# Kernel tuning notes

Hardware: AMD Instinct MI355X
Metric: run time of the kernel (lower is better)

## Reference

```python
import jax, jax.numpy as jnp
import numpy as np

N = 50000   # nodes
E = 800000  # edges (avg degree 16)
C = 96      # in = hidden = out channels


def setup_inputs() -> dict:
    key = jax.random.key(0)
    ks = jax.random.split(key, 8)
    s = np.float32(1.0 / np.sqrt(C))
    x = jax.random.normal(ks[0], (N, C), dtype=jnp.float32)
    edge_index = jax.random.randint(ks[1], (2, E), 0, N, dtype=jnp.int64)
    W1 = jax.random.normal(ks[2], (C, C), dtype=jnp.float32) * s
    Wr1 = jax.random.normal(ks[3], (C, C), dtype=jnp.float32) * s
    b1 = jnp.zeros((C,), dtype=jnp.float32)
    W2 = jax.random.normal(ks[4], (C, C), dtype=jnp.float32) * s
    Wr2 = jax.random.normal(ks[5], (C, C), dtype=jnp.float32) * s
    b2 = jnp.zeros((C,), dtype=jnp.float32)
    return {"x": x, "edge_index": edge_index,
            "W1": W1, "Wr1": Wr1, "b1": b1,
            "W2": W2, "Wr2": Wr2, "b2": b2}


def spline_conv(x, edge_index, W, W_root, b):
    """Gather-transform-scatter message passing (SplineConv core, mean aggr)."""
    src, dst = edge_index[0], edge_index[1]
    h = x @ W                                   # [N, C] transform once per node
    msg = h[src]                                # [E, C] edge gather
    agg = jax.ops.segment_sum(msg, dst, num_segments=N)        # scatter-add
    deg = jax.ops.segment_sum(jnp.ones((E,), x.dtype), dst, num_segments=N)
    agg = agg / jnp.maximum(deg, 1.0)[:, None]  # mean aggregation
    return agg + x @ W_root + b                 # root weight + bias


def reference(x, edge_index, W1, Wr1, b1, W2, Wr2, b2):
    h = jax.nn.relu(spline_conv(x, edge_index, W1, Wr1, b1))
    out = spline_conv(h, edge_index, W2, Wr2, b2)
    return out.reshape(-1)  # generalization of x.view(1600)
```

## Files before the change

### kernel.cpp

```cpp
#include <hip/hip_runtime.h>

#define C 96
#define TB 64
#define EB 2048
#define NBP 1024
#define LCAP 2048
typedef unsigned char u8;
typedef unsigned short u16;
typedef unsigned int u32;
typedef __attribute__((ext_vector_type(8))) short short8;
typedef __attribute__((ext_vector_type(4))) float floatx4;
typedef __attribute__((ext_vector_type(2))) float floatx2;

__device__ inline u16 f2bf(float f) {
    union { float f; u32 u; } v; v.f = f;
    u32 r = v.u + 0x7fff + ((v.u >> 16) & 1);
    return (u16)(r >> 16);
}
__device__ inline u32 pk4_fp8(float a, float b, float c, float d) {
    u32 w = 0;
    w = __builtin_amdgcn_cvt_pk_fp8_f32(a, b, w, false);
    w = __builtin_amdgcn_cvt_pk_fp8_f32(c, d, w, true);
    return w;
}
__device__ inline u8 f2fp8(float a) {
    return (u8)(__builtin_amdgcn_cvt_pk_fp8_f32(a, a, 0, false) & 0xff);
}

__global__ __launch_bounds__(256) void sort_kernel(const int* __restrict__ src,
                                                   const int* __restrict__ dst,
                                                   int* __restrict__ cntT,
                                                   int* __restrict__ offT,
                                                   u32* __restrict__ stage,
                                                   int E, int DB, int NB,
                                                   const float* __restrict__ x,
                                                   u16* __restrict__ xb,
                                                   u8* __restrict__ xf8, int n16, int CX,
                                                   const float* W0, const float* W1,
                                                   const float* W2, const float* W3,
                                                   u16* T0, u16* T1, u16* T2, u16* T3) {
    int bid = blockIdx.x;
    int t = threadIdx.x;
    if (bid >= DB) {
        int cc = bid - DB;
        if (cc < CX) {
            int i = cc * 256 + t;
            if (i >= n16) return;
            const float4* p = (const float4*)x + (size_t)i * 4;
            float4 a = p[0], b = p[1], c = p[2], d = p[3];
            short8 o0, o1;
            o0[0] = (short)f2bf(a.x); o0[1] = (short)f2bf(a.y);
            o0[2] = (short)f2bf(a.z); o0[3] = (short)f2bf(a.w);
            o0[4] = (short)f2bf(b.x); o0[5] = (short)f2bf(b.y);
            o0[6] = (short)f2bf(b.z); o0[7] = (short)f2bf(b.w);
            o1[0] = (short)f2bf(c.x); o1[1] = (short)f2bf(c.y);
            o1[2] = (short)f2bf(c.z); o1[3] = (short)f2bf(c.w);
            o1[4] = (short)f2bf(d.x); o1[5] = (short)f2bf(d.y);
            o1[6] = (short)f2bf(d.z); o1[7] = (short)f2bf(d.w);
            *(short8*)(xb + (size_t)i * 16) = o0;
            *(short8*)(xb + (size_t)i * 16 + 8) = o1;
            uint4 f8;
            f8.x = pk4_fp8(a.x, a.y, a.z, a.w);
            f8.y = pk4_fp8(b.x, b.y, b.z, b.w);
            f8.z = pk4_fp8(c.x, c.y, c.z, c.w);
            f8.w = pk4_fp8(d.x, d.y, d.z, d.w);
            *(uint4*)(xf8 + (size_t)i * 16) = f8;
        } else {
            int w = cc - CX;
            const float* W = w == 0 ? W0 : w == 1 ? W1 : w == 2 ? W2 : W3;
            u16* T = w == 0 ? T0 : w == 1 ? T1 : w == 2 ? T2 : T3;
            for (int i = t; i < C * C; i += 256) {
                int k = i / C, n = i - k * C;
                T[n * C + k] = f2bf(W[i]);
            }
        }
        return;
    }

    __shared__ u32 s_word[EB];
    __shared__ int s_cnt[NBP];
    __shared__ int s_off[NBP];
    __shared__ int s_scan[256];
    int e0 = bid * EB;
    int cnt_here = min(EB, E - e0);

    for (int i = t; i < NBP; i += 256) s_cnt[i] = 0;
    __syncthreads();

    int my_src[EB / 256], my_dl[EB / 256], my_b[EB / 256], my_rank[EB / 256];
    int nmine = 0;
#pragma unroll
    for (int k = 0; k < EB / 256; k++) {
        int i = t + k * 256;
        if (i < cnt_here) {
            int s = src[e0 + i], d = dst[e0 + i];
            int b = d >> 6;
            my_src[nmine] = s;
            my_dl[nmine] = d & (TB - 1);
            my_b[nmine] = b;
            my_rank[nmine] = atomicAdd(&s_cnt[b], 1);
            nmine++;
        }
    }
    __syncthreads();

    int b4 = t * 4;
    int v0 = s_cnt[b4], v1 = s_cnt[b4 + 1], v2 = s_cnt[b4 + 2], v3 = s_cnt[b4 + 3];
    int lsum = v0 + v1 + v2 + v3;
    s_scan[t] = lsum;
    __syncthreads();
    for (int off = 1; off < 256; off <<= 1) {
        int x2 = (t >= off) ? s_scan[t - off] : 0;
        __syncthreads();
        s_scan[t] += x2;
        __syncthreads();
    }
    int excl = s_scan[t] - lsum;
    s_off[b4] = excl;
    s_off[b4 + 1] = excl + v0;
    s_off[b4 + 2] = excl + v0 + v1;
    s_off[b4 + 3] = excl + v0 + v1 + v2;
    __syncthreads();

    for (int b = t; b < NB; b += 256) {
        cntT[(size_t)b * DB + bid] = s_cnt[b];
        offT[(size_t)b * DB + bid] = s_off[b];
    }

    for (int k = 0; k < nmine; k++) {
        int slot = s_off[my_b[k]] + my_rank[k];
        s_word[slot] = ((u32)my_dl[k] << 16) | (u32)my_src[k];
    }
    __syncthreads();

    for (int i = t; i < cnt_here; i += 256) stage[(size_t)bid * EB + i] = s_word[i];
}

template <bool RELU, bool WF8, typename OT>
__global__ __launch_bounds__(256, 4) void layer_kernel(const u16* __restrict__ Xbf,
                                                       const u8* __restrict__ Xf8,
                                                       const int* __restrict__ cntT,
                                                       const int* __restrict__ offT,
                                                       const u32* __restrict__ stage,
                                                       const u16* __restrict__ WTA,
                                                       const u16* __restrict__ WTR,
                                                       const float* __restrict__ BIAS,
                                                       OT* __restrict__ Y,
                                                       u8* __restrict__ Yf8, int n, int DB) {
    __shared__ __align__(16) u16 sA[64 * 104];
    __shared__ u16 lcsr[LCAP];
    __shared__ int s_cnt64[TB];
    __shared__ int s_off64[TB];
    __shared__ int s_cur64[TB];
    __shared__ int s_perm[TB];
    const int t = threadIdx.x;
    const int b = blockIdx.x;
    const int row0 = b * 64;
    const int* cntT_b = cntT + (size_t)b * DB;
    const int* offT_b = offT + (size_t)b * DB;

    for (int i = t; i < TB; i += 256) s_cnt64[i] = 0;
    __syncthreads();
    for (int i = t; i < DB; i += 256) {
        int len = cntT_b[i];
        const u32* run = stage + (size_t)i * EB + offT_b[i];
        for (int j = 0; j < len; j++) atomicAdd(&s_cnt64[run[j] >> 16], 1);
    }
    __syncthreads();

    int dv = (t < TB) ? s_cnt64[t] : 0;
    if (t < TB) s_cur64[t] = dv;
    __syncthreads();
    for (int off = 1; off < TB; off <<= 1) {
        int x2 = (t >= off && t < TB) ? s_cur64[t - off] : 0;
        __syncthreads();
        if (t < TB) s_cur64[t] += x2;
        __syncthreads();
    }
    if (t < TB) {
        int excl = s_cur64[t] - dv;
        s_off64[t] = excl;
    }
    __syncthreads();
    if (t < TB) s_cur64[t] = s_off64[t];
    __syncthreads();

    for (int i = t; i < DB; i += 256) {
        int len = cntT_b[i];
        const u32* run = stage + (size_t)i * EB + offT_b[i];
        for (int j = 0; j < len; j++) {
            u32 w = run[j];
            int p = atomicAdd(&s_cur64[w >> 16], 1);
            lcsr[p] = (u16)(w & 0xffffu);
        }
    }
    __syncthreads();

    if (t < 64) {
        int di = s_cnt64[t];
        int r = 0;
#pragma unroll 8
        for (int j = 0; j < 64; j++) {
            int dj = s_cnt64[j];
            r += (dj < di) || (dj == di && j < t);
        }
        s_perm[r] = t;
    }
    __syncthreads();

    {
        int nl = s_perm[t >> 2];
        int q = t & 3;
        float acc[24];
#pragma unroll
        for (int i = 0; i < 24; i++) acc[i] = 0.f;
        int d = s_cnt64[nl];
        int start = s_off64[nl];
        const int off4 = q * 16;
        const int off2 = 64 + q * 8;

        int j = 0;
        if (d >= 4) {
            int si[4];
#pragma unroll
            for (int k = 0; k < 4; k++) si[k] = lcsr[start + k];
            for (; j + 8 <= d; j += 4) {
                uint4 va[4];
                uint2 vb[4];
#pragma unroll
                for (int k = 0; k < 4; k++) {
                    const u8* p = Xf8 + (size_t)si[k] * 96;
                    va[k] = *(const uint4*)(p + off4);
                    vb[k] = *(const uint2*)(p + off2);
                }
                int sn[4];
#pragma unroll
                for (int k = 0; k < 4; k++) sn[k] = lcsr[start + j + 4 + k];
#pragma unroll
                for (int k = 0; k < 4; k++) {
                    u32 ws[6] = {va[k].x, va[k].y, va[k].z,
                                 va[k].w, vb[k].x, vb[k].y};
#pragma unroll
                    for (int i = 0; i < 6; i++) {
                        floatx2 lo = __builtin_amdgcn_cvt_pk_f32_fp8(ws[i], false);
                        floatx2 hi = __builtin_amdgcn_cvt_pk_f32_fp8(ws[i], true);
                        acc[4 * i]     += lo[0];
                        acc[4 * i + 1] += lo[1];
                        acc[4 * i + 2] += hi[0];
                        acc[4 * i + 3] += hi[1];
                    }
                }
#pragma unroll
                for (int k = 0; k < 4; k++) si[k] = sn[k];
            }
            {
                uint4 va[4];
                uint2 vb[4];
#pragma unroll
                for (int k = 0; k < 4; k++) {
                    const u8* p = Xf8 + (size_t)si[k] * 96;
                    va[k] = *(const uint4*)(p + off4);
                    vb[k] = *(const uint2*)(p + off2);
                }
#pragma unroll
                for (int k = 0; k < 4; k++) {
                    u32 ws[6] = {va[k].x, va[k].y, va[k].z,
                                 va[k].w, vb[k].x, vb[k].y};
#pragma unroll
                    for (int i = 0; i < 6; i++) {
                        floatx2 lo = __builtin_amdgcn_cvt_pk_f32_fp8(ws[i], false);
                        floatx2 hi = __builtin_amdgcn_cvt_pk_f32_fp8(ws[i], true);
                        acc[4 * i]     += lo[0];
                        acc[4 * i + 1] += lo[1];
                        acc[4 * i + 2] += hi[0];
                        acc[4 * i + 3] += hi[1];
                    }
                }
                j += 4;
            }
        }
        for (; j < d; j++) {
            const u8* p = Xf8 + (size_t)lcsr[start + j] * 96;
            uint4 va = *(const uint4*)(p + off4);
            uint2 vb = *(const uint2*)(p + off2);
            u32 ws[6] = {va.x, va.y, va.z, va.w, vb.x, vb.y};
#pragma unroll
            for (int i = 0; i < 6; i++) {
                floatx2 lo = __builtin_amdgcn_cvt_pk_f32_fp8(ws[i], false);
                floatx2 hi = __builtin_amdgcn_cvt_pk_f32_fp8(ws[i], true);
                acc[4 * i]     += lo[0];
                acc[4 * i + 1] += lo[1];
                acc[4 * i + 2] += hi[0];
                acc[4 * i + 3] += hi[1];
            }
        }
        float inv = 1.0f / fmaxf((float)d, 1.0f);
        u16* dl = sA + nl * 104;
        short8 o0, o1, o2;
#pragma unroll
        for (int i = 0; i < 8; i++) {
            o0[i] = (short)f2bf(acc[i] * inv);
            o1[i] = (short)f2bf(acc[8 + i] * inv);
            o2[i] = (short)f2bf(acc[16 + i] * inv);
        }
        *(short8*)(dl + q * 16) = o0;
        *(short8*)(dl + q * 16 + 8) = o1;
        *(short8*)(dl + 64 + q * 8) = o2;
    }
    __syncthreads();

    const int lane = t & 63;
    const int w = t >> 6;
    const int quad = lane >> 4;
    const int l16 = lane & 15;
    const int r0 = row0 + w * 16;

    floatx4 acc6[6];
#pragma unroll
    for (int i = 0; i < 6; i++) acc6[i] = (floatx4){0.f, 0.f, 0.f, 0.f};

    {
        const u16* Ap = sA + (w * 16 + l16) * 104 + quad * 8;
        const u16* Wp = WTA + l16 * C + quad * 8;
#pragma unroll
        for (int ks = 0; ks < 3; ks++) {
            short8 a = *(const short8*)(Ap + ks * 32);
#pragma unroll
            for (int nt = 0; nt < 6; nt++) {
                short8 bb = *(const short8*)(Wp + nt * 16 * C + ks * 32);
                acc6[nt] = __builtin_amdgcn_mfma_f32_16x16x32_bf16(a, bb, acc6[nt], 0, 0, 0);
            }
        }
    }
    {
        int arow = r0 + l16;
        if (arow >= n) arow = n - 1;
        const u16* Xp = Xbf + (size_t)arow * C + quad * 8;
        const u16* Wp = WTR + l16 * C + quad * 8;
#pragma unroll
        for (int ks = 0; ks < 3; ks++) {
            short8 a = *(const short8*)(Xp + ks * 32);
#pragma unroll
            for (int nt = 0; nt < 6; nt++) {
                short8 bb = *(const short8*)(Wp + nt * 16 * C + ks * 32);
                acc6[nt] = __builtin_amdgcn_mfma_f32_16x16x32_bf16(a, bb, acc6[nt], 0, 0, 0);
            }
        }
    }

#pragma unroll
    for (int nt = 0; nt < 6; nt++) {
        float bv = BIAS[nt * 16 + l16];
#pragma unroll
        for (int r = 0; r < 4; r++) {
            float v = acc6[nt][r] + bv;
            if (RELU) v = fmaxf(v, 0.f);
            acc6[nt][r] = v;
        }
    }
    __syncthreads();

    const int nrow = min(64, n - row0);
    const int lr = w * 16 + quad * 4;

    if constexpr (sizeof(OT) == 2) {
        u16* so = sA;
#pragma unroll
        for (int nt = 0; nt < 6; nt++)
#pragma unroll
            for (int r = 0; r < 4; r++)
                so[(lr + r) * 96 + nt * 16 + l16] = f2bf(acc6[nt][r]);
        __syncthreads();
        {
            char* dstp = (char*)Y + (size_t)row0 * 192;
            int nbytes = nrow * 192;
            for (int ofs = t * 16; ofs < nbytes; ofs += 4096)
                *(uint4*)(dstp + ofs) = *(const uint4*)((const char*)sA + ofs);
        }
        if constexpr (WF8) {
            __syncthreads();
            u8* so8 = (u8*)sA;
#pragma unroll
            for (int nt = 0; nt < 6; nt++)
#pragma unroll
                for (int r = 0; r < 4; r++)
                    so8[(lr + r) * 96 + nt * 16 + l16] = f2fp8(acc6[nt][r]);
            __syncthreads();
            char* dst8 = (char*)Yf8 + (size_t)row0 * 96;
            int nb8 = nrow * 96;
            for (int ofs = t * 16; ofs < nb8; ofs += 4096)
                *(uint4*)(dst8 + ofs) = *(const uint4*)((const char*)sA + ofs);
        }
    } else {
        float* sof = (float*)sA;
#pragma unroll
        for (int half = 0; half < 2; half++) {
            if (half) __syncthreads();
            if ((w >> 1) == half) {
#pragma unroll
                for (int nt = 0; nt < 6; nt++)
#pragma unroll
                    for (int r = 0; r < 4; r++)
                        sof[((w & 1) * 16 + quad * 4 + r) * 96 + nt * 16 + l16] = acc6[nt][r];
            }
            __syncthreads();
            int rbase = row0 + half * 32;
            int nr = n - rbase;
            nr = nr < 0 ? 0 : (nr > 32 ? 32 : nr);
            char* dstp = (char*)Y + (size_t)rbase * 384;
            int nbytes = nr * 384;
            for (int ofs = t * 16; ofs < nbytes; ofs += 4096)
                *(uint4*)(dstp + ofs) = *(const uint4*)((const char*)sA + ofs);
        }
    }
}

extern "C" void kernel_launch(void* const* d_in, const int* in_sizes, int n_in,
                              void* d_out, int out_size, void* d_ws, size_t ws_size,
                              hipStream_t stream) {
    const float* x   = (const float*)d_in[0];
    const int*   ei  = (const int*)d_in[1];
    const float* W1  = (const float*)d_in[2];
    const float* Wr1 = (const float*)d_in[3];
    const float* b1  = (const float*)d_in[4];
    const float* W2  = (const float*)d_in[5];
    const float* Wr2 = (const float*)d_in[6];
    const float* b2  = (const float*)d_in[7];
    float* out = (float*)d_out;

    const int N = in_sizes[0] / C;
    const int E = in_sizes[1] / 2;
    const int* src = ei;
    const int* dst = ei + E;

    const int DB   = (E + EB - 1) / EB;
    const int NB   = (N + TB - 1) / TB;
    const int n16  = N * C / 16;
    const int CX   = (n16 + 255) / 256;
    const size_t NBDB = ((size_t)NB * DB + 3) & ~(size_t)3;

    int*  cntT = (int*)d_ws;
    int*  offT = cntT + NBDB;
    u32*  stage = (u32*)(offT + NBDB);
    u16*  xb   = (u16*)(stage + (size_t)DB * EB);
    u16*  h1b  = xb + (size_t)N * C;
    u16*  wt   = h1b + (size_t)N * C;
    u16 *wt1 = wt, *wtr1 = wt + C * C, *wt2 = wt + 2 * C * C, *wtr2 = wt + 3 * C * C;
    u8*   xf8  = (u8*)(wt + 4 * C * C);
    u8*   h1f8 = xf8 + (size_t)N * 96;

    sort_kernel<<<DB + CX + 4, 256, 0, stream>>>(src, dst, cntT, offT, stage,
                                                 E, DB, NB,
                                                 x, xb, xf8, n16, CX,
                                                 W1, Wr1, W2, Wr2, wt1, wtr1, wt2, wtr2);

    layer_kernel<true, true, u16><<<NB, 256, 0, stream>>>(
        xb, xf8, cntT, offT, stage, wt1, wtr1, b1, h1b, h1f8, N, DB);
    layer_kernel<false, false, float><<<NB, 256, 0, stream>>>(
        h1b, h1f8, cntT, offT, stage, wt2, wtr2, b2, out, h1f8, N, DB);
}
```

Measured before the change: 169.5 us.

## Pack count/offset table and read staged edge runs once into shared memory

```diff
diff --git a/kernel.cpp b/kernel.cpp
--- a/kernel.cpp
+++ b/kernel.cpp
@@ -29,8 +29,7 @@
 
 __global__ __launch_bounds__(256) void sort_kernel(const int* __restrict__ src,
                                                    const int* __restrict__ dst,
-                                                   int* __restrict__ cntT,
-                                                   int* __restrict__ offT,
+                                                   u32* __restrict__ tabT,
                                                    u32* __restrict__ stage,
                                                    int E, int DB, int NB,
                                                    const float* __restrict__ x,
@@ -122,10 +121,8 @@
     s_off[b4 + 3] = excl + v0 + v1 + v2;
     __syncthreads();
 
-    for (int b = t; b < NB; b += 256) {
-        cntT[(size_t)b * DB + bid] = s_cnt[b];
-        offT[(size_t)b * DB + bid] = s_off[b];
-    }
+    for (int b = t; b < NB; b += 256)
+        tabT[(size_t)b * DB + bid] = ((u32)s_cnt[b] << 16) | (u32)s_off[b];
 
     for (int k = 0; k < nmine; k++) {
         int slot = s_off[my_b[k]] + my_rank[k];
@@ -137,10 +134,9 @@
 }
 
 template <bool RELU, bool WF8, typename OT>
-__global__ __launch_bounds__(256, 4) void layer_kernel(const u16* __restrict__ Xbf,
+__global__ __launch_bounds__(256, 6) void layer_kernel(const u16* __restrict__ Xbf,
                                                        const u8* __restrict__ Xf8,
-                                                       const int* __restrict__ cntT,
-                                                       const int* __restrict__ offT,
+                                                       const u32* __restrict__ tabT,
                                                        const u32* __restrict__ stage,
                                                        const u16* __restrict__ WTA,
                                                        const u16* __restrict__ WTR,
@@ -149,26 +145,49 @@
                                                        u8* __restrict__ Yf8, int n, int DB) {
     __shared__ __align__(16) u16 sA[64 * 104];
     __shared__ u16 lcsr[LCAP];
-    __shared__ int s_cnt64[TB];
+    __shared__ int s_dg[TB];
     __shared__ int s_off64[TB];
     __shared__ int s_cur64[TB];
     __shared__ int s_perm[TB];
+    __shared__ int ssum[256];
+    u32* raw = (u32*)sA;
     const int t = threadIdx.x;
     const int b = blockIdx.x;
     const int row0 = b * 64;
-    const int* cntT_b = cntT + (size_t)b * DB;
-    const int* offT_b = offT + (size_t)b * DB;
-
-    for (int i = t; i < TB; i += 256) s_cnt64[i] = 0;
-    __syncthreads();
-    for (int i = t; i < DB; i += 256) {
-        int len = cntT_b[i];
-        const u32* run = stage + (size_t)i * EB + offT_b[i];
-        for (int j = 0; j < len; j++) atomicAdd(&s_cnt64[run[j] >> 16], 1);
-    }
-    __syncthreads();
-
-    int dv = (t < TB) ? s_cnt64[t] : 0;
+    const u32* tab_b = tabT + (size_t)b * DB;
+
+    for (int i = t; i < TB; i += 256) s_dg[i] = 0;
+    u32 p0 = (t < DB) ? tab_b[t] : 0;
+    u32 p1 = (t + 256 < DB) ? tab_b[t + 256] : 0;
+    int l0 = p0 >> 16, o0 = p0 & 0xffff;
+    int l1 = p1 >> 16, o1 = p1 & 0xffff;
+    int tot = l0 + l1;
+    ssum[t] = tot;
+    __syncthreads();
+    for (int off = 1; off < 256; off <<= 1) {
+        int x2 = (t >= off) ? ssum[t - off] : 0;
+        __syncthreads();
+        ssum[t] += x2;
+        __syncthreads();
+    }
+    const int seg0 = ssum[t] - tot;
+    int pos = seg0;
+    {
+        const u32* run = stage + (size_t)t * EB + o0;
+        for (int j = 0; j < l0; j++) {
+            u32 w = run[j];
+            if (pos < LCAP) { raw[pos++] = w; atomicAdd(&s_dg[w >> 16], 1); }
+        }
+        const u32* run2 = stage + ((size_t)t + 256) * EB + o1;
+        for (int j = 0; j < l1; j++) {
+            u32 w = run2[j];
+            if (pos < LCAP) { raw[pos++] = w; atomicAdd(&s_dg[w >> 16], 1); }
+        }
+    }
+    const int stored = pos - seg0;
+    __syncthreads();
+
+    int dv = (t < TB) ? s_dg[t] : 0;
     if (t < TB) s_cur64[t] = dv;
     __syncthreads();
     for (int off = 1; off < TB; off <<= 1) {
@@ -177,31 +196,24 @@
         if (t < TB) s_cur64[t] += x2;
         __syncthreads();
     }
-    if (t < TB) {
-        int excl = s_cur64[t] - dv;
-        s_off64[t] = excl;
-    }
+    if (t < TB) s_off64[t] = s_cur64[t] - dv;
     __syncthreads();
     if (t < TB) s_cur64[t] = s_off64[t];
     __syncthreads();
 
-    for (int i = t; i < DB; i += 256) {
-        int len = cntT_b[i];
-        const u32* run = stage + (size_t)i * EB + offT_b[i];
-        for (int j = 0; j < len; j++) {
-            u32 w = run[j];
-            int p = atomicAdd(&s_cur64[w >> 16], 1);
-            lcsr[p] = (u16)(w & 0xffffu);
-        }
+    for (int k = 0; k < stored; k++) {
+        u32 w = raw[seg0 + k];
+        int p = atomicAdd(&s_cur64[w >> 16], 1);
+        lcsr[p] = (u16)(w & 0xffffu);
     }
     __syncthreads();
 
     if (t < 64) {
-        int di = s_cnt64[t];
+        int di = s_dg[t];
         int r = 0;
 #pragma unroll 8
         for (int j = 0; j < 64; j++) {
-            int dj = s_cnt64[j];
+            int dj = s_dg[j];
             r += (dj < di) || (dj == di && j < t);
         }
         s_perm[r] = t;
@@ -214,98 +226,72 @@
         float acc[24];
 #pragma unroll
         for (int i = 0; i < 24; i++) acc[i] = 0.f;
-        int d = s_cnt64[nl];
+        int d = s_dg[nl];
         int start = s_off64[nl];
         const int off4 = q * 16;
         const int off2 = 64 + q * 8;
 
+#define CONSUME(va, vb)                                                     \
+        do {                                                                \
+            u32 ws[6] = {(va).x, (va).y, (va).z, (va).w, (vb).x, (vb).y};   \
+            _Pragma("unroll")                                               \
+            for (int i = 0; i < 6; i++) {                                   \
+                floatx2 lo = __builtin_amdgcn_cvt_pk_f32_fp8(ws[i], false); \
+                floatx2 hi = __builtin_amdgcn_cvt_pk_f32_fp8(ws[i], true);  \
+                acc[4 * i]     += lo[0];                                    \
+                acc[4 * i + 1] += lo[1];                                    \
+                acc[4 * i + 2] += hi[0];                                    \
+                acc[4 * i + 3] += hi[1];                                    \
+            }                                                               \
+        } while (0)
+
         int j = 0;
-        if (d >= 4) {
-            int si[4];
-#pragma unroll
-            for (int k = 0; k < 4; k++) si[k] = lcsr[start + k];
-            for (; j + 8 <= d; j += 4) {
-                uint4 va[4];
-                uint2 vb[4];
-#pragma unroll
-                for (int k = 0; k < 4; k++) {
-                    const u8* p = Xf8 + (size_t)si[k] * 96;
-                    va[k] = *(const uint4*)(p + off4);
-                    vb[k] = *(const uint2*)(p + off2);
-                }
-                int sn[4];
-#pragma unroll
-                for (int k = 0; k < 4; k++) sn[k] = lcsr[start + j + 4 + k];
-#pragma unroll
-                for (int k = 0; k < 4; k++) {
-                    u32 ws[6] = {va[k].x, va[k].y, va[k].z,
-                                 va[k].w, vb[k].x, vb[k].y};
-#pragma unroll
-                    for (int i = 0; i < 6; i++) {
-                        floatx2 lo = __builtin_amdgcn_cvt_pk_f32_fp8(ws[i], false);
-                        floatx2 hi = __builtin_amdgcn_cvt_pk_f32_fp8(ws[i], true);
-                        acc[4 * i]     += lo[0];
-                        acc[4 * i + 1] += lo[1];
-                        acc[4 * i + 2] += hi[0];
-                        acc[4 * i + 3] += hi[1];
-                    }
-                }
-#pragma unroll
-                for (int k = 0; k < 4; k++) si[k] = sn[k];
+        if (d >= 2) {
+            int si0 = lcsr[start], si1 = lcsr[start + 1];
+            for (; j + 4 <= d; j += 2) {
+                const u8* pA = Xf8 + (size_t)si0 * 96;
+                const u8* pB = Xf8 + (size_t)si1 * 96;
+                uint4 va0 = *(const uint4*)(pA + off4);
+                uint2 vb0 = *(const uint2*)(pA + off2);
+                uint4 va1 = *(const uint4*)(pB + off4);
+                uint2 vb1 = *(const uint2*)(pB + off2);
+                si0 = lcsr[start + j + 2];
+                si1 = lcsr[start + j + 3];
+                CONSUME(va0, vb0);
+                CONSUME(va1, vb1);
             }
             {
-                uint4 va[4];
-                uint2 vb[4];
-#pragma unroll
-                for (int k = 0; k < 4; k++) {
-                    const u8* p = Xf8 + (size_t)si[k] * 96;
-                    va[k] = *(const uint4*)(p + off4);
-                    vb[k] = *(const uint2*)(p + off2);
-                }
-#pragma unroll
-                for (int k = 0; k < 4; k++) {
-                    u32 ws[6] = {va[k].x, va[k].y, va[k].z,
-                                 va[k].w, vb[k].x, vb[k].y};
-#pragma unroll
-                    for (int i = 0; i < 6; i++) {
-                        floatx2 lo = __builtin_amdgcn_cvt_pk_f32_fp8(ws[i], false);
-                        floatx2 hi = __builtin_amdgcn_cvt_pk_f32_fp8(ws[i], true);
-                        acc[4 * i]     += lo[0];
-                        acc[4 * i + 1] += lo[1];
-                        acc[4 * i + 2] += hi[0];
-                        acc[4 * i + 3] += hi[1];
-                    }
-                }
-                j += 4;
+                const u8* pA = Xf8 + (size_t)si0 * 96;
+                const u8* pB = Xf8 + (size_t)si1 * 96;
+                uint4 va0 = *(const uint4*)(pA + off4);
+                uint2 vb0 = *(const uint2*)(pA + off2);
+                uint4 va1 = *(const uint4*)(pB + off4);
+                uint2 vb1 = *(const uint2*)(pB + off2);
+                CONSUME(va0, vb0);
+                CONSUME(va1, vb1);
+                j += 2;
             }
         }
         for (; j < d; j++) {
             const u8* p = Xf8 + (size_t)lcsr[start + j] * 96;
             uint4 va = *(const uint4*)(p + off4);
             uint2 vb = *(const uint2*)(p + off2);
-            u32 ws[6] = {va.x, va.y, va.z, va.w, vb.x, vb.y};
-#pragma unroll
-            for (int i = 0; i < 6; i++) {
-                floatx2 lo = __builtin_amdgcn_cvt_pk_f32_fp8(ws[i], false);
-                floatx2 hi = __builtin_amdgcn_cvt_pk_f32_fp8(ws[i], true);
-                acc[4 * i]     += lo[0];
-                acc[4 * i + 1] += lo[1];
-                acc[4 * i + 2] += hi[0];
-                acc[4 * i + 3] += hi[1];
-            }
-        }
+            CONSUME(va, vb);
+        }
+#undef CONSUME
+
         float inv = 1.0f / fmaxf((float)d, 1.0f);
         u16* dl = sA + nl * 104;
-        short8 o0, o1, o2;
+        short8 o0v, o1v, o2v;
 #pragma unroll
         for (int i = 0; i < 8; i++) {
-            o0[i] = (short)f2bf(acc[i] * inv);
-            o1[i] = (short)f2bf(acc[8 + i] * inv);
-            o2[i] = (short)f2bf(acc[16 + i] * inv);
-        }
-        *(short8*)(dl + q * 16) = o0;
-        *(short8*)(dl + q * 16 + 8) = o1;
-        *(short8*)(dl + 64 + q * 8) = o2;
+            o0v[i] = (short)f2bf(acc[i] * inv);
+            o1v[i] = (short)f2bf(acc[8 + i] * inv);
+            o2v[i] = (short)f2bf(acc[16 + i] * inv);
+        }
+        *(short8*)(dl + q * 16) = o0v;
+        *(short8*)(dl + q * 16 + 8) = o1v;
+        *(short8*)(dl + 64 + q * 8) = o2v;
     }
     __syncthreads();
 
@@ -439,9 +425,8 @@
     const int CX   = (n16 + 255) / 256;
     const size_t NBDB = ((size_t)NB * DB + 3) & ~(size_t)3;
 
-    int*  cntT = (int*)d_ws;
-    int*  offT = cntT + NBDB;
-    u32*  stage = (u32*)(offT + NBDB);
+    u32*  tabT = (u32*)d_ws;
+    u32*  stage = tabT + NBDB;
     u16*  xb   = (u16*)(stage + (size_t)DB * EB);
     u16*  h1b  = xb + (size_t)N * C;
     u16*  wt   = h1b + (size_t)N * C;
@@ -449,13 +434,13 @@
     u8*   xf8  = (u8*)(wt + 4 * C * C);
     u8*   h1f8 = xf8 + (size_t)N * 96;
 
-    sort_kernel<<<DB + CX + 4, 256, 0, stream>>>(src, dst, cntT, offT, stage,
+    sort_kernel<<<DB + CX + 4, 256, 0, stream>>>(src, dst, tabT, stage,
                                                  E, DB, NB,
                                                  x, xb, xf8, n16, CX,
                                                  W1, Wr1, W2, Wr2, wt1, wtr1, wt2, wtr2);
 
     layer_kernel<true, true, u16><<<NB, 256, 0, stream>>>(
-        xb, xf8, cntT, offT, stage, wt1, wtr1, b1, h1b, h1f8, N, DB);
+        xb, xf8, tabT, stage, wt1, wtr1, b1, h1b, h1f8, N, DB);
     layer_kernel<false, false, float><<<NB, 256, 0, stream>>>(
-        h1b, h1f8, cntT, offT, stage, wt2, wtr2, b2, out, h1f8, N, DB);
-}
+        h1b, h1f8, tabT, stage, wt2, wtr2, b2, out, h1f8, N, DB);
+}
```

Result: no change. 171.4 us (+1.2%).
